# Kernel tuning notes

Measured on AMD Instinct MI355X. Metric: run time of the kernel, lower is better.

The kernel has to match this reference:

```python
import jax, jax.numpy as jnp
import numpy as np

DIM = 1024
B, T = 4, 8192


def setup_inputs() -> dict:
    key = jax.random.key(0)
    ks = jax.random.split(key, 5)
    scale = 1.0 / np.sqrt(DIM)
    x = jax.random.normal(ks[0], (B, T, DIM), dtype=jnp.float32)
    w_in = jax.random.uniform(ks[1], (DIM, DIM), jnp.float32, -scale, scale)
    b_in = jax.random.uniform(ks[2], (DIM,), jnp.float32, -scale, scale)
    a = jnp.zeros((DIM,), jnp.float32)   # nn.Parameter(torch.zeros(dim))
    b = jnp.ones((DIM,), jnp.float32)    # nn.Parameter(torch.ones(dim))
    w_out = jax.random.uniform(ks[3], (DIM, DIM), jnp.float32, -scale, scale)
    b_out = jax.random.uniform(ks[4], (DIM,), jnp.float32, -scale, scale)
    return {"x": x, "w_in": w_in, "b_in": b_in, "a": a, "b": b,
            "w_out": w_out, "b_out": b_out}


def reference(x, w_in, b_in, a, b, w_out, b_out):
    # h = in_proj(x): [B, T, D]
    h = jnp.einsum('btd,ed->bte', x, w_in) + b_in
    A = jax.nn.sigmoid(a)  # [D], diagonal transition

    def step(state, h_t):
        state = A * state + b * h_t  # [B, D]
        return state, state

    init = jnp.zeros_like(h[:, 0])  # [B, D]
    _, ys = jax.lax.scan(step, init, jnp.swapaxes(h, 0, 1))  # ys: [T, B, D]
    y = jnp.swapaxes(ys, 0, 1)  # [B, T, D]
    return jnp.einsum('btd,ed->bte', y, w_out) + b_out
```

## Files before the change

### kernel.cpp

```cpp
#include <hip/hip_runtime.h>
#include <hip/hip_bf16.h>
#include <cstdint>

#define DIM 1024
#define BATCH 4
#define SEQ 8192
#define M_TOTAL (BATCH * SEQ)

#define CH 64
#define CL (SEQ / CH)

using bf16 = __hip_bfloat16;
typedef __attribute__((ext_vector_type(4))) float f32x4;
typedef __attribute__((ext_vector_type(8))) __bf16 bf16x8;

#define NT (DIM / 64)
#define NI (NT / 2)

#define BAR()      __builtin_amdgcn_s_barrier()
#define LGKM0()    asm volatile("s_waitcnt lgkmcnt(0)")
#define WAIT_VM(n) asm volatile("s_waitcnt vmcnt(" #n ")")

__global__ void convert_all(const float* __restrict__ x, bf16* __restrict__ xb,
                            const float* __restrict__ w1, bf16* __restrict__ w1b,
                            const float* __restrict__ w2, bf16* __restrict__ w2b,
                            long n4x, long n4w) {
    long i = blockIdx.x * (long)blockDim.x + threadIdx.x;
    const float* in;
    bf16* out;
    long off;
    if (i < n4x)              { in = x;  out = xb;  off = i; }
    else if (i < n4x + n4w)   { in = w1; out = w1b; off = i - n4x; }
    else if (i < n4x + 2*n4w) { in = w2; out = w2b; off = i - n4x - n4w; }
    else return;
    const float4 v = ((const float4*)in)[off];
    __hip_bfloat162* o = (__hip_bfloat162*)(out + off * 4);
    o[0] = __float22bfloat162_rn(make_float2(v.x, v.y));
    o[1] = __float22bfloat162_rn(make_float2(v.z, v.w));
}

__device__ __forceinline__ void stage_half(const bf16* __restrict__ g,
                                           char* ldsbase, int tid) {
    const int w = tid >> 6, l = tid & 63;
    const int kc = (l & 7) ^ ((l >> 3) & 7);
#pragma unroll
    for (int j = 0; j < 2; j++) {
        const int idx = (w * 2 + j) * 64 + l;
        const int row = w * 16 + j * 8 + (l >> 3);
        const bf16* src = g + (size_t)row * DIM + kc * 8;
        __builtin_amdgcn_global_load_lds(
            (const __attribute__((address_space(1))) void*)src,
            (__attribute__((address_space(3))) void*)(ldsbase + idx * 16),
            16, 0, 0);
    }
}

template <int OUT_MODE>
__global__ __launch_bounds__(512, 2) void gemm256(
    const bf16* __restrict__ A, const bf16* __restrict__ B,
    const float* __restrict__ bias, void* __restrict__ C,
    const float* __restrict__ acoef, const float* __restrict__ bcoef,
    float* __restrict__ S) {
    __shared__ __align__(16) char lds[131072];

    const int tid  = threadIdx.x;
    const int wave = tid >> 6;
    const int l    = tid & 63;

    const int orig = blockIdx.x;
    const int xcd  = orig & 7;
    const int li   = orig >> 3;
    const int bm   = xcd * 16 + (li >> 2);
    const int bn   = li & 3;

    const bf16* Abase = A + (size_t)bm * 256 * DIM;
    const bf16* Bbase = B + (size_t)bn * 256 * DIM;

    char* pa0 = lds + (wave >> 2) * 16384;
    char* pb0 = lds + 32768 + ((wave & 3) >> 1) * 16384 + (wave & 1) * 8192;
    char* pa1 = pa0 + 65536;
    char* pb1 = pb0 + 65536;

    const int rl = l & 15;
    const int lg = l >> 4;
    const int r7 = l & 7;
    const int ao0 = rl * 128 + ((lg ^ r7) << 4);
    const int ao1 = rl * 128 + (((4 + lg) ^ r7) << 4);

    f32x4 acc[8][4];
#pragma unroll
    for (int m = 0; m < 8; m++)
#pragma unroll
        for (int n = 0; n < 4; n++)
#pragma unroll
            for (int r = 0; r < 4; r++) acc[m][n][r] = 0.f;

    bf16x8 af[4][2], bfr[4][2];

#define READ_A4(PA, FMB)                                                   \
    _Pragma("unroll") for (int m_ = 0; m_ < 4; m_++) {                     \
        af[m_][0] = *(const bf16x8*)((PA) + (FMB + m_) * 2048 + ao0);      \
        af[m_][1] = *(const bf16x8*)((PA) + (FMB + m_) * 2048 + ao1);      \
    }
#define READ_B2(PB, FNB)                                                   \
    _Pragma("unroll") for (int n_ = 0; n_ < 2; n_++) {                     \
        bfr[FNB + n_][0] = *(const bf16x8*)((PB) + (FNB + n_) * 2048 + ao0); \
        bfr[FNB + n_][1] = *(const bf16x8*)((PB) + (FNB + n_) * 2048 + ao1); \
    }
#define MFMA16(MB, NB2)                                                    \
    __builtin_amdgcn_s_setprio(1);                                         \
    _Pragma("unroll") for (int m_ = 0; m_ < 4; m_++)                       \
    _Pragma("unroll") for (int n_ = 0; n_ < 2; n_++)                       \
    _Pragma("unroll") for (int k_ = 0; k_ < 2; k_++)                       \
        acc[MB + m_][NB2 + n_] = __builtin_amdgcn_mfma_f32_16x16x32_bf16(  \
            af[m_][k_], bfr[NB2 + n_][k_], acc[MB + m_][NB2 + n_], 0, 0, 0); \
    __builtin_amdgcn_s_setprio(0);

    stage_half(Abase,                          lds +     0, tid);
    stage_half(Abase + (size_t)128 * DIM,      lds + 16384, tid);
    stage_half(Bbase,                          lds + 32768, tid);
    stage_half(Bbase + (size_t)128 * DIM,      lds + 49152, tid);
    stage_half(Bbase + 64,                     lds + 65536 + 32768, tid);
    stage_half(Bbase + (size_t)128 * DIM + 64, lds + 65536 + 49152, tid);
    WAIT_VM(4);
    BAR();

    for (int i = 0; i < NI; ++i) {
        const bool last = (i == NI - 1);
        const size_t kt1 = (size_t)(2 * i + 1) * 64;
        const size_t kt2 = kt1 + 64;
        const size_t kt3 = kt1 + 128;

        READ_A4(pa0, 0); READ_B2(pb0, 0);
        stage_half(Abase + kt1, lds + 65536, tid);
        BAR(); LGKM0(); MFMA16(0, 0); BAR();

        READ_B2(pb0, 2);
        stage_half(Abase + (size_t)128 * DIM + kt1, lds + 65536 + 16384, tid);
        BAR(); LGKM0(); MFMA16(0, 2); BAR();

        READ_A4(pa0, 4);
        if (!last) stage_half(Bbase + kt2, lds + 32768, tid);
        BAR(); LGKM0(); MFMA16(4, 0); BAR();

        if (!last)
            stage_half(Bbase + (size_t)128 * DIM + kt2, lds + 49152, tid);
        BAR(); LGKM0(); MFMA16(4, 2);
        if (last) { WAIT_VM(0); } else { WAIT_VM(4); }
        BAR();

        READ_A4(pa1, 0); READ_B2(pb1, 0);
        if (!last) stage_half(Abase + kt2, lds + 0, tid);
        BAR(); LGKM0(); MFMA16(0, 0); BAR();

        READ_B2(pb1, 2);
        if (!last) stage_half(Abase + (size_t)128 * DIM + kt2, lds + 16384, tid);
        BAR(); LGKM0(); MFMA16(0, 2); BAR();

        READ_A4(pa1, 4);
        if (!last) stage_half(Bbase + kt3, lds + 65536 + 32768, tid);
        BAR(); LGKM0(); MFMA16(4, 0); BAR();

        if (!last)
            stage_half(Bbase + (size_t)128 * DIM + kt3, lds + 65536 + 49152, tid);
        BAR(); LGKM0(); MFMA16(4, 2);
        if (!last) { WAIT_VM(4); }
        BAR();
    }

    const int wm = (wave >> 2) * 128;
    const int wn = (wave & 3) * 64;
    const long mb = (long)bm * 256 + wm;
    const int nb = bn * 256 + wn;
    const int crow = lg * 4;

    float bv[4];
#pragma unroll
    for (int n = 0; n < 4; n++) bv[n] = bias[nb + n * 16 + rl];

    if (OUT_MODE == 1) {
        float* O = (float*)C;
#pragma unroll
        for (int m = 0; m < 8; m++)
#pragma unroll
            for (int n = 0; n < 4; n++) {
                const int col = nb + n * 16 + rl;
#pragma unroll
                for (int r = 0; r < 4; r++)
                    O[(mb + m * 16 + crow + r) * (long)DIM + col] =
                        acc[m][n][r] + bv[n];
            }
    } else {
        bf16* H = (bf16*)C;
#pragma unroll
        for (int m = 0; m < 8; m++)
#pragma unroll
            for (int n = 0; n < 4; n++) {
                const int col  = nb + n * 16 + rl;
                const int lcol = wn + n * 16 + rl;
#pragma unroll
                for (int r = 0; r < 4; r++) {
                    const int lrow = wm + m * 16 + crow + r;
                    const bf16 hv = __float2bfloat16(acc[m][n][r] + bv[n]);
                    H[(mb + m * 16 + crow + r) * (long)DIM + col] = hv;
                    const int cb = (lcol * 2) ^ (((lrow >> 2) & 7) << 4);
                    *(bf16*)(lds + lrow * 512 + cb) = hv;
                }
            }
        __syncthreads();
        const int c   = tid & 255;
        const int ch2 = tid >> 8;
        const int d   = bn * 256 + c;
        const float Ad = 1.f / (1.f + expf(-acoef[d]));
        const float bd = bcoef[d];
        float s = 0.f;
#pragma unroll 8
        for (int t = 0; t < CL; t++) {
            const int lrow = ch2 * 128 + t;
            const int cb = (c * 2) ^ (((lrow >> 2) & 7) << 4);
            const float v = __bfloat162float(*(const bf16*)(lds + lrow * 512 + cb));
            s = Ad * s + bd * v;
        }
        S[((long)bm * 2 + ch2) * DIM + d] = s;
    }
#undef READ_A4
#undef READ_B2
#undef MFMA16
}

__global__ __launch_bounds__(512) void scan_pass3(
    bf16* __restrict__ h, const float* __restrict__ a,
    const float* __restrict__ bcoef, const float* __restrict__ S) {
    const int d2 = threadIdx.x;
    const int blk = blockIdx.x;
    const int b = blk / CH, c = blk % CH;
    const float A0 = 1.f / (1.f + expf(-a[2 * d2]));
    const float A1 = 1.f / (1.f + expf(-a[2 * d2 + 1]));
    const float b0 = bcoef[2 * d2];
    const float b1 = bcoef[2 * d2 + 1];
    float Ap0 = A0, Ap1 = A1;
#pragma unroll
    for (int i = 0; i < 7; i++) { Ap0 *= Ap0; Ap1 *= Ap1; }

    float c0 = 0.f, c1 = 0.f;
    const float2* Sp = (const float2*)(S + (long)b * CH * DIM) + d2;
    for (int i0 = 0; i0 < c; i0 += 8) {
        float2 sv[8];
        int nn = (c - i0 < 8) ? (c - i0) : 8;
#pragma unroll 8
        for (int j = 0; j < 8; j++)
            if (j < nn) sv[j] = Sp[(long)(i0 + j) * (DIM / 2)];
#pragma unroll 8
        for (int j = 0; j < 8; j++)
            if (j < nn) { c0 = Ap0 * c0 + sv[j].x; c1 = Ap1 * c1 + sv[j].y; }
    }

    float s0 = c0, s1 = c1;
    __hip_bfloat162* hp =
        (__hip_bfloat162*)(h + ((long)b * SEQ + (long)c * CL) * DIM) + d2;
#pragma unroll 8
    for (int t = 0; t < CL; t++) {
        float2 v = __bfloat1622float2(hp[(long)t * (DIM / 2)]);
        s0 = A0 * s0 + b0 * v.x;
        s1 = A1 * s1 + b1 * v.y;
        hp[(long)t * (DIM / 2)] = __float22bfloat162_rn(make_float2(s0, s1));
    }
}

extern "C" void kernel_launch(void* const* d_in, const int* in_sizes, int n_in,
                              void* d_out, int out_size, void* d_ws,
                              size_t ws_size, hipStream_t stream) {
    const float* x     = (const float*)d_in[0];
    const float* w_in  = (const float*)d_in[1];
    const float* b_in  = (const float*)d_in[2];
    const float* a     = (const float*)d_in[3];
    const float* bcoef = (const float*)d_in[4];
    const float* w_out = (const float*)d_in[5];
    const float* b_out = (const float*)d_in[6];
    float* out = (float*)d_out;

    char* ws = (char*)d_ws;
    bf16* xb  = (bf16*)ws;  ws += (size_t)M_TOTAL * DIM * 2;
    bf16* wib = (bf16*)ws;  ws += (size_t)DIM * DIM * 2;
    bf16* wob = (bf16*)ws;  ws += (size_t)DIM * DIM * 2;
    bf16* h   = (bf16*)ws;  ws += (size_t)M_TOTAL * DIM * 2;
    float* S  = (float*)ws; ws += (size_t)BATCH * CH * DIM * 4;

    {
        long n4x = (long)M_TOTAL * DIM / 4;
        long n4w = (long)DIM * DIM / 4;
        long total = n4x + 2 * n4w;
        convert_all<<<(int)((total + 255) / 256), 256, 0, stream>>>(
            x, xb, w_in, wib, w_out, wob, n4x, n4w);
    }

    const int nblocks = (M_TOTAL / 256) * (DIM / 256);

    gemm256<0><<<nblocks, 512, 0, stream>>>(xb, wib, b_in, h, a, bcoef, S);

    scan_pass3<<<BATCH * CH, 512, 0, stream>>>(h, a, bcoef, S);

    gemm256<1><<<nblocks, 512, 0, stream>>>(h, wob, b_out, out,
                                            nullptr, nullptr, nullptr);
}
```

Baseline: 382.4 us.

## Fuse x conversion and chunk-carry fixup into GEMM A-operand loading

Removes the separate fp32-to-bf16 conversion of x. The first GEMM now loads fp32 x directly, converts it in registers and writes it to LDS. The first GEMM's epilogue now writes the chunk-local scan output instead of raw h. The scan_pass3 pass that reread and rewrote h is replaced by a tiny carry/power kernel, and the second GEMM applies y + A^k·carry while staging its A operand. This cuts several full passes over the 32K×1024 activation tensor, but the A loads change from async global-to-LDS copies to register round trips, which adds VGPR pressure and more load traffic (fp32 x, plus powA and carry per tile).

```diff
diff --git a/kernel.cpp b/kernel.cpp
--- a/kernel.cpp
+++ b/kernel.cpp
@@ -14,25 +14,21 @@
 typedef __attribute__((ext_vector_type(4))) float f32x4;
 typedef __attribute__((ext_vector_type(8))) __bf16 bf16x8;
 
-#define NT (DIM / 64)
-#define NI (NT / 2)
+#define NI 8
 
 #define BAR()      __builtin_amdgcn_s_barrier()
 #define LGKM0()    asm volatile("s_waitcnt lgkmcnt(0)")
 #define WAIT_VM(n) asm volatile("s_waitcnt vmcnt(" #n ")")
-
-__global__ void convert_all(const float* __restrict__ x, bf16* __restrict__ xb,
-                            const float* __restrict__ w1, bf16* __restrict__ w1b,
-                            const float* __restrict__ w2, bf16* __restrict__ w2b,
-                            long n4x, long n4w) {
-    long i = blockIdx.x * (long)blockDim.x + threadIdx.x;
-    const float* in;
-    bf16* out;
-    long off;
-    if (i < n4x)              { in = x;  out = xb;  off = i; }
-    else if (i < n4x + n4w)   { in = w1; out = w1b; off = i - n4x; }
-    else if (i < n4x + 2*n4w) { in = w2; out = w2b; off = i - n4x - n4w; }
-    else return;
+#define GLOAD(D, P) asm volatile("global_load_dwordx4 %0, %1, off" : "=v"(D) : "v"(P))
+#define DSW(A, V)   asm volatile("ds_write_b128 %0, %1" :: "v"(A), "v"(V))
+
+__global__ void convert_w(const float* __restrict__ w1, bf16* __restrict__ o1,
+                          const float* __restrict__ w2, bf16* __restrict__ o2) {
+    const long n4 = (long)DIM * DIM / 4;
+    long i = blockIdx.x * 256L + threadIdx.x;
+    const float* in; bf16* out; long off;
+    if (i < n4) { in = w1; out = o1; off = i; }
+    else        { in = w2; out = o2; off = i - n4; }
     const float4 v = ((const float4*)in)[off];
     __hip_bfloat162* o = (__hip_bfloat162*)(out + off * 4);
     o[0] = __float22bfloat162_rn(make_float2(v.x, v.y));
@@ -55,13 +51,35 @@
     }
 }
 
-template <int OUT_MODE>
+__device__ __forceinline__ f32x4 cvt8(f32x4 a, f32x4 b) {
+    bf16x8 r;
+#pragma unroll
+    for (int i = 0; i < 4; i++) { r[i] = (__bf16)a[i]; r[4 + i] = (__bf16)b[i]; }
+    return __builtin_bit_cast(f32x4, r);
+}
+__device__ __forceinline__ f32x4 fix8(f32x4 yv, f32x4 plo, f32x4 phi,
+                                      f32x4 clo, f32x4 chi) {
+    bf16x8 y = __builtin_bit_cast(bf16x8, yv);
+    bf16x8 r;
+#pragma unroll
+    for (int i = 0; i < 4; i++) {
+        r[i]     = (__bf16)((float)y[i]     + plo[i] * clo[i]);
+        r[4 + i] = (__bf16)((float)y[4 + i] + phi[i] * chi[i]);
+    }
+    return __builtin_bit_cast(f32x4, r);
+}
+
+template <int MODE>
 __global__ __launch_bounds__(512, 2) void gemm256(
-    const bf16* __restrict__ A, const bf16* __restrict__ B,
+    const void* __restrict__ Asrc, const bf16* __restrict__ B,
     const float* __restrict__ bias, void* __restrict__ C,
     const float* __restrict__ acoef, const float* __restrict__ bcoef,
-    float* __restrict__ S) {
+    float* __restrict__ S, const float* __restrict__ powA,
+    const float* __restrict__ carry) {
     __shared__ __align__(16) char lds[131072];
+
+    const float* Xf = (const float*)Asrc;
+    const bf16*  Yb = (const bf16*)Asrc;
 
     const int tid  = threadIdx.x;
     const int wave = tid >> 6;
@@ -73,7 +91,6 @@
     const int bm   = xcd * 16 + (li >> 2);
     const int bn   = li & 3;
 
-    const bf16* Abase = A + (size_t)bm * 256 * DIM;
     const bf16* Bbase = B + (size_t)bn * 256 * DIM;
 
     char* pa0 = lds + (wave >> 2) * 16384;
@@ -86,6 +103,59 @@
     const int r7 = l & 7;
     const int ao0 = rl * 128 + ((lg ^ r7) << 4);
     const int ao1 = rl * 128 + (((4 + lg) ^ r7) << 4);
+
+    const int kcn  = l & 7;
+    const int r8   = l >> 3;
+    const int slot = kcn ^ r8;
+    const int rA0  = wave * 16 + r8;
+    const int colA = kcn * 8;
+    const unsigned ldsb32 =
+        (unsigned)(uintptr_t)(__attribute__((address_space(3))) char*)lds;
+    const unsigned dsoff0 = (unsigned)(rA0 * 128 + slot * 16);
+    const unsigned dsoff1 = dsoff0 + 1024;
+
+    f32x4 xa00a, xa00b, xa01a, xa01b, xa10a, xa10b, xa11a, xa11b;
+    f32x4 ya00, ya01, ya10, ya11;
+    f32x4 pa00a, pa00b, pa01a, pa01b, pa10a, pa10b, pa11a, pa11b;
+    f32x4 ca0a, ca0b, ca1a, ca1b;
+
+#define A_ISSUE(Sl, KT, RH) do {                                              \
+    if constexpr (MODE == 1) {                                                \
+        const float* p_ = Xf + ((size_t)(bm * 256 + (RH) * 128 + rA0)) * DIM  \
+                          + (KT) + colA;                                      \
+        GLOAD(xa##Sl##0a, p_);           GLOAD(xa##Sl##0b, p_ + 4);           \
+        GLOAD(xa##Sl##1a, p_ + 8 * DIM); GLOAD(xa##Sl##1b, p_ + 8 * DIM + 4); \
+    } else {                                                                  \
+        const bf16* y_ = Yb + ((size_t)(bm * 256 + (RH) * 128 + rA0)) * DIM   \
+                         + (KT) + colA;                                       \
+        const float* pw_ = powA + (size_t)rA0 * DIM + (KT) + colA;            \
+        const float* cw_ = carry + (size_t)(bm * 2 + (RH)) * DIM + (KT) + colA; \
+        GLOAD(ya##Sl##0, y_); GLOAD(ya##Sl##1, y_ + 8 * DIM);                 \
+        GLOAD(pa##Sl##0a, pw_);           GLOAD(pa##Sl##0b, pw_ + 4);         \
+        GLOAD(pa##Sl##1a, pw_ + 8 * DIM); GLOAD(pa##Sl##1b, pw_ + 8 * DIM + 4); \
+        GLOAD(ca##Sl##a, cw_);            GLOAD(ca##Sl##b, cw_ + 4);          \
+    } } while (0)
+
+#define A_WW(Sl, N1, N2, DSB) do {                                            \
+    if constexpr (MODE == 1) {                                                \
+        asm volatile("s_waitcnt vmcnt(" N1 ")"                                \
+            : "+v"(xa##Sl##0a), "+v"(xa##Sl##0b),                             \
+              "+v"(xa##Sl##1a), "+v"(xa##Sl##1b));                            \
+        f32x4 t0_ = cvt8(xa##Sl##0a, xa##Sl##0b);                             \
+        f32x4 t1_ = cvt8(xa##Sl##1a, xa##Sl##1b);                             \
+        DSW(ldsb32 + (DSB) + dsoff0, t0_);                                    \
+        DSW(ldsb32 + (DSB) + dsoff1, t1_);                                    \
+    } else {                                                                  \
+        asm volatile("s_waitcnt vmcnt(" N2 ")"                                \
+            : "+v"(ya##Sl##0), "+v"(ya##Sl##1),                               \
+              "+v"(pa##Sl##0a), "+v"(pa##Sl##0b),                             \
+              "+v"(pa##Sl##1a), "+v"(pa##Sl##1b),                             \
+              "+v"(ca##Sl##a), "+v"(ca##Sl##b));                              \
+        f32x4 t0_ = fix8(ya##Sl##0, pa##Sl##0a, pa##Sl##0b, ca##Sl##a, ca##Sl##b); \
+        f32x4 t1_ = fix8(ya##Sl##1, pa##Sl##1a, pa##Sl##1b, ca##Sl##a, ca##Sl##b); \
+        DSW(ldsb32 + (DSB) + dsoff0, t0_);                                    \
+        DSW(ldsb32 + (DSB) + dsoff1, t1_);                                    \
+    } } while (0)
 
     f32x4 acc[8][4];
 #pragma unroll
@@ -116,56 +186,65 @@
             af[m_][k_], bfr[NB2 + n_][k_], acc[MB + m_][NB2 + n_], 0, 0, 0); \
     __builtin_amdgcn_s_setprio(0);
 
-    stage_half(Abase,                          lds +     0, tid);
-    stage_half(Abase + (size_t)128 * DIM,      lds + 16384, tid);
+    A_ISSUE(0, 0, 0);
+    A_ISSUE(1, 0, 1);
     stage_half(Bbase,                          lds + 32768, tid);
     stage_half(Bbase + (size_t)128 * DIM,      lds + 49152, tid);
     stage_half(Bbase + 64,                     lds + 65536 + 32768, tid);
     stage_half(Bbase + (size_t)128 * DIM + 64, lds + 65536 + 49152, tid);
+    A_WW(0, "8", "8", 0);
+    A_WW(1, "8", "8", 16384);
+    LGKM0();
     WAIT_VM(4);
     BAR();
 
     for (int i = 0; i < NI; ++i) {
         const bool last = (i == NI - 1);
-        const size_t kt1 = (size_t)(2 * i + 1) * 64;
-        const size_t kt2 = kt1 + 64;
-        const size_t kt3 = kt1 + 128;
+        const int kt1 = (2 * i + 1) * 64;
+        const int kt2 = kt1 + 64;
+        const int kt3 = kt1 + 128;
 
         READ_A4(pa0, 0); READ_B2(pb0, 0);
-        stage_half(Abase + kt1, lds + 65536, tid);
+        A_ISSUE(0, kt1, 0);
         BAR(); LGKM0(); MFMA16(0, 0); BAR();
 
         READ_B2(pb0, 2);
-        stage_half(Abase + (size_t)128 * DIM + kt1, lds + 65536 + 16384, tid);
+        A_ISSUE(1, kt1, 1);
         BAR(); LGKM0(); MFMA16(0, 2); BAR();
 
         READ_A4(pa0, 4);
+        A_WW(0, "4", "8", 65536);
         if (!last) stage_half(Bbase + kt2, lds + 32768, tid);
-        BAR(); LGKM0(); MFMA16(4, 0); BAR();
-
-        if (!last)
+        LGKM0(); BAR(); MFMA16(4, 0); BAR();
+
+        if (!last) {
+            A_WW(1, "2", "2", 65536 + 16384);
             stage_half(Bbase + (size_t)128 * DIM + kt2, lds + 49152, tid);
-        BAR(); LGKM0(); MFMA16(4, 2);
-        if (last) { WAIT_VM(0); } else { WAIT_VM(4); }
-        BAR();
+        } else {
+            A_WW(1, "0", "0", 65536 + 16384);
+        }
+        LGKM0(); BAR(); MFMA16(4, 2); BAR();
 
         READ_A4(pa1, 0); READ_B2(pb1, 0);
-        if (!last) stage_half(Abase + kt2, lds + 0, tid);
+        if (!last) A_ISSUE(0, kt2, 0);
         BAR(); LGKM0(); MFMA16(0, 0); BAR();
 
         READ_B2(pb1, 2);
-        if (!last) stage_half(Abase + (size_t)128 * DIM + kt2, lds + 16384, tid);
+        if (!last) A_ISSUE(1, kt2, 1);
         BAR(); LGKM0(); MFMA16(0, 2); BAR();
 
         READ_A4(pa1, 4);
-        if (!last) stage_half(Bbase + kt3, lds + 65536 + 32768, tid);
-        BAR(); LGKM0(); MFMA16(4, 0); BAR();
-
-        if (!last)
+        if (!last) {
+            A_WW(0, "4", "8", 0);
+            stage_half(Bbase + kt3, lds + 65536 + 32768, tid);
+        }
+        LGKM0(); BAR(); MFMA16(4, 0); BAR();
+
+        if (!last) {
+            A_WW(1, "2", "2", 16384);
             stage_half(Bbase + (size_t)128 * DIM + kt3, lds + 65536 + 49152, tid);
-        BAR(); LGKM0(); MFMA16(4, 2);
-        if (!last) { WAIT_VM(4); }
-        BAR();
+        }
+        LGKM0(); BAR(); MFMA16(4, 2); BAR();
     }
 
     const int wm = (wave >> 2) * 128;
@@ -178,7 +257,7 @@
 #pragma unroll
     for (int n = 0; n < 4; n++) bv[n] = bias[nb + n * 16 + rl];
 
-    if (OUT_MODE == 1) {
+    if constexpr (MODE == 2) {
         float* O = (float*)C;
 #pragma unroll
         for (int m = 0; m < 8; m++)
@@ -191,18 +270,14 @@
                         acc[m][n][r] + bv[n];
             }
     } else {
-        bf16* H = (bf16*)C;
-#pragma unroll
         for (int m = 0; m < 8; m++)
 #pragma unroll
             for (int n = 0; n < 4; n++) {
-                const int col  = nb + n * 16 + rl;
                 const int lcol = wn + n * 16 + rl;
 #pragma unroll
                 for (int r = 0; r < 4; r++) {
                     const int lrow = wm + m * 16 + crow + r;
                     const bf16 hv = __float2bfloat16(acc[m][n][r] + bv[n]);
-                    H[(mb + m * 16 + crow + r) * (long)DIM + col] = hv;
                     const int cb = (lcol * 2) ^ (((lrow >> 2) & 7) << 4);
                     *(bf16*)(lds + lrow * 512 + cb) = hv;
                 }
@@ -213,57 +288,53 @@
         const int d   = bn * 256 + c;
         const float Ad = 1.f / (1.f + expf(-acoef[d]));
         const float bd = bcoef[d];
+        bf16* Yo = (bf16*)C;
+        const size_t rbase = (size_t)bm * 256 + (size_t)ch2 * 128;
         float s = 0.f;
 #pragma unroll 8
         for (int t = 0; t < CL; t++) {
             const int lrow = ch2 * 128 + t;
             const int cb = (c * 2) ^ (((lrow >> 2) & 7) << 4);
-            const float v = __bfloat162float(*(const bf16*)(lds + lrow * 512 + cb));
+            const float v =
+                __bfloat162float(*(const bf16*)(lds + lrow * 512 + cb));
             s = Ad * s + bd * v;
-        }
-        S[((long)bm * 2 + ch2) * DIM + d] = s;
-    }
+            Yo[(rbase + t) * DIM + d] = __float2bfloat16(s);
+        }
+        S[((size_t)bm * 2 + ch2) * DIM + d] = s;
+    }
+#undef A_ISSUE
+#undef A_WW
 #undef READ_A4
 #undef READ_B2
 #undef MFMA16
 }
 
-__global__ __launch_bounds__(512) void scan_pass3(
-    bf16* __restrict__ h, const float* __restrict__ a,
-    const float* __restrict__ bcoef, const float* __restrict__ S) {
-    const int d2 = threadIdx.x;
-    const int blk = blockIdx.x;
-    const int b = blk / CH, c = blk % CH;
-    const float A0 = 1.f / (1.f + expf(-a[2 * d2]));
-    const float A1 = 1.f / (1.f + expf(-a[2 * d2 + 1]));
-    const float b0 = bcoef[2 * d2];
-    const float b1 = bcoef[2 * d2 + 1];
-    float Ap0 = A0, Ap1 = A1;
-#pragma unroll
-    for (int i = 0; i < 7; i++) { Ap0 *= Ap0; Ap1 *= Ap1; }
-
-    float c0 = 0.f, c1 = 0.f;
-    const float2* Sp = (const float2*)(S + (long)b * CH * DIM) + d2;
-    for (int i0 = 0; i0 < c; i0 += 8) {
-        float2 sv[8];
-        int nn = (c - i0 < 8) ? (c - i0) : 8;
-#pragma unroll 8
-        for (int j = 0; j < 8; j++)
-            if (j < nn) sv[j] = Sp[(long)(i0 + j) * (DIM / 2)];
-#pragma unroll 8
-        for (int j = 0; j < 8; j++)
-            if (j < nn) { c0 = Ap0 * c0 + sv[j].x; c1 = Ap1 * c1 + sv[j].y; }
-    }
-
-    float s0 = c0, s1 = c1;
-    __hip_bfloat162* hp =
-        (__hip_bfloat162*)(h + ((long)b * SEQ + (long)c * CL) * DIM) + d2;
-#pragma unroll 8
-    for (int t = 0; t < CL; t++) {
-        float2 v = __bfloat1622float2(hp[(long)t * (DIM / 2)]);
-        s0 = A0 * s0 + b0 * v.x;
-        s1 = A1 * s1 + b1 * v.y;
-        hp[(long)t * (DIM / 2)] = __float22bfloat162_rn(make_float2(s0, s1));
+__global__ __launch_bounds__(512) void carry_powA(
+    const float* __restrict__ a, const float* __restrict__ S,
+    float* __restrict__ carry, float* __restrict__ powA) {
+    if (blockIdx.x < 8) {
+        const int idx = blockIdx.x * 512 + threadIdx.x;
+        const int b = idx >> 10, d = idx & 1023;
+        const float A = 1.f / (1.f + expf(-a[d]));
+        float Ap = A;
+#pragma unroll
+        for (int i = 0; i < 7; i++) Ap *= Ap;
+        float acc = 0.f;
+        for (int c = 0; c < CH; c++) {
+            const size_t g = (size_t)b * CH + c;
+            carry[g * DIM + d] = acc;
+            acc = Ap * acc + S[g * DIM + d];
+        }
+    } else {
+        const int d = (blockIdx.x - 8) * 512 + threadIdx.x;
+        if (d < DIM) {
+            const float A = 1.f / (1.f + expf(-a[d]));
+            float p = A;
+            for (int k = 0; k < CL; k++) {
+                powA[(size_t)k * DIM + d] = p;
+                p *= A;
+            }
+        }
     }
 }
 
@@ -280,26 +351,22 @@
     float* out = (float*)d_out;
 
     char* ws = (char*)d_ws;
-    bf16* xb  = (bf16*)ws;  ws += (size_t)M_TOTAL * DIM * 2;
-    bf16* wib = (bf16*)ws;  ws += (size_t)DIM * DIM * 2;
-    bf16* wob = (bf16*)ws;  ws += (size_t)DIM * DIM * 2;
-    bf16* h   = (bf16*)ws;  ws += (size_t)M_TOTAL * DIM * 2;
-    float* S  = (float*)ws; ws += (size_t)BATCH * CH * DIM * 4;
-
-    {
-        long n4x = (long)M_TOTAL * DIM / 4;
-        long n4w = (long)DIM * DIM / 4;
-        long total = n4x + 2 * n4w;
-        convert_all<<<(int)((total + 255) / 256), 256, 0, stream>>>(
-            x, xb, w_in, wib, w_out, wob, n4x, n4w);
-    }
+    bf16*  wib   = (bf16*)ws;  ws += (size_t)DIM * DIM * 2;
+    bf16*  wob   = (bf16*)ws;  ws += (size_t)DIM * DIM * 2;
+    bf16*  Ybuf  = (bf16*)ws;  ws += (size_t)M_TOTAL * DIM * 2;
+    float* S     = (float*)ws; ws += (size_t)BATCH * CH * DIM * 4;
+    float* carry = (float*)ws; ws += (size_t)BATCH * CH * DIM * 4;
+    float* powA  = (float*)ws; ws += (size_t)CL * DIM * 4;
+
+    convert_w<<<2048, 256, 0, stream>>>(w_in, wib, w_out, wob);
 
     const int nblocks = (M_TOTAL / 256) * (DIM / 256);
 
-    gemm256<0><<<nblocks, 512, 0, stream>>>(xb, wib, b_in, h, a, bcoef, S);
-
-    scan_pass3<<<BATCH * CH, 512, 0, stream>>>(h, a, bcoef, S);
-
-    gemm256<1><<<nblocks, 512, 0, stream>>>(h, wob, b_out, out,
-                                            nullptr, nullptr, nullptr);
-}
+    gemm256<1><<<nblocks, 512, 0, stream>>>(x, wib, b_in, Ybuf, a, bcoef, S,
+                                            nullptr, nullptr);
+
+    carry_powA<<<10, 512, 0, stream>>>(a, S, carry, powA);
+
+    gemm256<2><<<nblocks, 512, 0, stream>>>(Ybuf, wob, b_out, out, nullptr,
+                                            nullptr, nullptr, powA, carry);
+}
```

Result: slower. 664.1 us (+73.7%).
